# Performance work log

Hardware: AMD Instinct MI355X
Metric: run time of the kernel (lower is better)

The kernel has to match this reference:

```python
import jax, jax.numpy as jnp
import numpy as np

K, B, L, D_IN, H = 4, 16, 4096, 512, 128

def setup_inputs() -> dict:
    key = jax.random.key(0)
    k1, k2, k3, k4, k5 = jax.random.split(key, 5)
    hs = jax.random.normal(k1, (K, B, L, D_IN), dtype=jnp.float32)
    mask = jax.random.randint(k2, (B, L), 0, 2, dtype=jnp.int32)
    # xavier-ish scaled params
    ln_w = jax.random.normal(k3, (H, D_IN + H), dtype=jnp.float32) * (1.0 / np.sqrt(D_IN + H))
    ln_b = jnp.zeros((H,), dtype=jnp.float32)
    v_w = jax.random.normal(k4, (H,), dtype=jnp.float32) * (1.0 / np.sqrt(H))
    vq = jax.random.normal(k5, (H,), dtype=jnp.float32) * (1.0 / np.sqrt(H))
    return {"hs": hs, "mask": mask, "ln_w": ln_w, "ln_b": ln_b, "v_w": v_w, "vq": vq}

def reference(hs, mask, ln_w, ln_b, v_w, vq):
    # hs: [K,B,L,D], mask: [B,L], ln_w: [H, D+H], vq/v_w/ln_b: [H]
    d = hs.shape[-1]
    W_h = ln_w[:, :d]        # [H, D]
    W_q = ln_w[:, d:]        # [H, H]
    # Linear over concat([hs, vq]) == hs @ W_h.T + W_q @ vq + b (vq is constant per position)
    q_bias = W_q @ vq + ln_b                      # [H]
    h = jnp.tanh(jnp.einsum('kbld,hd->kblh', hs, W_h) + q_bias)
    s = jnp.einsum('kblh,h->kbl', h, v_w)         # [K,B,L]
    s = s - (mask[None] == 0).astype(s.dtype) * 10000.0
    a = jax.nn.softmax(s, axis=0)                 # softmax over the K (stack) axis
    x = jnp.einsum('kbl,kbld->bld', a, hs)        # weighted sum over K
    return x  # dropout is identity in eval mode
```

## Files before the change

### kernel.cpp

```cpp
#include <hip/hip_runtime.h>
#include <hip/hip_bf16.h>
#include <stdint.h>

#define KK 4
#define BB 16
#define LL 4096
#define DD 512
#define HH 128

typedef __attribute__((ext_vector_type(8))) short bf16x8;
typedef __attribute__((ext_vector_type(4))) float f32x4;
typedef __attribute__((ext_vector_type(4))) unsigned int u32x4;

__device__ __forceinline__ unsigned int pack_bf16(float lo, float hi) {
  unsigned int a = __float_as_uint(lo);
  unsigned int b = __float_as_uint(hi);
  a = (a + 0x7FFFu + ((a >> 16) & 1u)) >> 16;
  b = (b + 0x7FFFu + ((b >> 16) & 1u)) >> 16;
  return a | (b << 16);
}

__device__ __forceinline__ void bar_lds() {
  __builtin_amdgcn_sched_barrier(0);
  asm volatile("s_waitcnt lgkmcnt(0)" ::: "memory");
  __builtin_amdgcn_s_barrier();
  __builtin_amdgcn_sched_barrier(0);
}

__global__ void qbias_kernel(const float* __restrict__ ln_w,
                             const float* __restrict__ ln_b,
                             const float* __restrict__ vq,
                             float* __restrict__ qb) {
  int h = threadIdx.x;
  if (h < HH) {
    float acc = ln_b[h];
    const float* wq = ln_w + (size_t)h * (DD + HH) + DD;
    for (int j = 0; j < HH; ++j) acc = fmaf(wq[j], vq[j], acc);
    qb[h] = acc;
  }
}

__global__ void wf_kernel(const float* __restrict__ ln_w,
                          unsigned int* __restrict__ wf) {
  int gid = blockIdx.x * 256 + threadIdx.x;
  int ks = gid >> 9;
  int nt = (gid >> 6) & 7;
  int lane = gid & 63;
  int h = nt * 16 + (lane & 15);
  int d0 = ks * 32 + (lane >> 4) * 8;
  const float* src = ln_w + (size_t)h * (DD + HH) + d0;
  u32x4 v;
  v.x = pack_bf16(src[0], src[1]);
  v.y = pack_bf16(src[2], src[3]);
  v.z = pack_bf16(src[4], src[5]);
  v.w = pack_bf16(src[6], src[7]);
  *(u32x4*)(wf + (size_t)gid * 4) = v;
}

__global__ __launch_bounds__(512) void agg_main(
    const float* __restrict__ hs, const unsigned int* __restrict__ wf,
    const float* __restrict__ qb, const float* __restrict__ vw,
    float* __restrict__ out) {
  extern __shared__ char smem[];
  char* abuf = smem;
  f32x4* spv = (f32x4*)(smem + 65536);

  const int tid = threadIdx.x;
  const int lane = tid & 63;
  const int wv = tid >> 6;
  const int r = lane & 15;
  const int cg = lane >> 4;

  const int b = blockIdx.x >> 4;
  const int l0b = (blockIdx.x & 15) << 8;

  bf16x8 wreg[16];
#pragma unroll
  for (int ks = 0; ks < 16; ++ks)
    wreg[ks] = *(const bf16x8*)(wf + ((size_t)((ks * 8 + wv) * 64 + lane)) * 4);

  const float qbr = qb[wv * 16 + r];
  const float vwr = vw[wv * 16 + r];

  f32x4 sv[8];
  auto issue_stage = [&](int l0) {
#pragma unroll
    for (int i = 0; i < 4; ++i) {
      int row = i * 8 + wv;
      int k = row & 3, pos = row >> 2;
      int d0 = (lane ^ (row & 7)) * 8;
      const float* p = hs + (((size_t)(k * BB + b)) * LL + l0 + pos) * DD + d0;
      sv[i * 2]     = *(const f32x4*)(p);
      sv[i * 2 + 1] = *(const f32x4*)(p + 4);
    }
  };
  auto write_stage = [&](char* dst) {
#pragma unroll
    for (int i = 0; i < 4; ++i) {
      u32x4 pk;
      pk.x = pack_bf16(sv[i * 2].x, sv[i * 2].y);
      pk.y = pack_bf16(sv[i * 2].z, sv[i * 2].w);
      pk.z = pack_bf16(sv[i * 2 + 1].x, sv[i * 2 + 1].y);
      pk.w = pack_bf16(sv[i * 2 + 1].z, sv[i * 2 + 1].w);
      *(u32x4*)(dst + i * 8192 + tid * 16) = pk;
    }
  };

  issue_stage(l0b);
  write_stage(abuf);
  bar_lds();

  for (int t = 0; t < 32; ++t) {
    const int l0 = l0b + t * 8;
    char* cur = abuf + (t & 1) * 32768;
    char* nxt = abuf + ((t & 1) ^ 1) * 32768;

    if (t < 31) issue_stage(l0 + 8);

    f32x4 acc0 = {0.f, 0.f, 0.f, 0.f};
    f32x4 acc1 = {0.f, 0.f, 0.f, 0.f};
    const int swz = (r & 7) << 4;
#pragma unroll
    for (int ks = 0; ks < 16; ++ks) {
      int inner = (ks * 64 + cg * 16) ^ swz;
      bf16x8 a0 = *(const bf16x8*)(cur + r * 1024 + inner);
      bf16x8 a1 = *(const bf16x8*)(cur + (16 + r) * 1024 + inner);
      acc0 = __builtin_amdgcn_mfma_f32_16x16x32_bf16(a0, wreg[ks], acc0, 0, 0, 0);
      acc1 = __builtin_amdgcn_mfma_f32_16x16x32_bf16(a1, wreg[ks], acc1, 0, 0, 0);
    }

    float ps[8];
#pragma unroll
    for (int st = 0; st < 2; ++st) {
      f32x4 acc = st ? acc1 : acc0;
#pragma unroll
      for (int j = 0; j < 4; ++j) {
        float z = acc[j] + qbr;
        z = fminf(15.f, fmaxf(-15.f, z));
        float e = __expf(-2.f * z);
        float th = (1.f - e) * __builtin_amdgcn_rcpf(1.f + e);
        ps[st * 4 + j] = vwr * th;
      }
    }
#pragma unroll
    for (int m = 1; m < 16; m <<= 1) {
#pragma unroll
      for (int q = 0; q < 8; ++q) ps[q] += __shfl_xor(ps[q], m, 64);
    }
    if (r == 0) {
      f32x4 v0 = {ps[0], ps[1], ps[2], ps[3]};
      f32x4 v1 = {ps[4], ps[5], ps[6], ps[7]};
      spv[cg * 8 + wv] = v0;
      spv[(4 + cg) * 8 + wv] = v1;
    }
    bar_lds();

    float a0, a1, a2, a3;
    {
      f32x4 s = spv[wv * 8 + 0];
#pragma unroll
      for (int w2 = 1; w2 < 8; ++w2) s += spv[wv * 8 + w2];
      float mx = fmaxf(fmaxf(s.x, s.y), fmaxf(s.z, s.w));
      float e0 = __expf(s.x - mx), e1 = __expf(s.y - mx);
      float e2 = __expf(s.z - mx), e3 = __expf(s.w - mx);
      float inv = __builtin_amdgcn_rcpf(e0 + e1 + e2 + e3);
      a0 = e0 * inv; a1 = e1 * inv; a2 = e2 * inv; a3 = e3 * inv;
    }

    {
      float x[8];
#pragma unroll
      for (int j = 0; j < 8; ++j) x[j] = 0.f;
#pragma unroll
      for (int k = 0; k < 4; ++k) {
        int row = wv * 4 + k;
        float ak = k == 0 ? a0 : (k == 1 ? a1 : (k == 2 ? a2 : a3));
        u32x4 u = *(const u32x4*)(cur + row * 1024 + ((lane * 16) ^ ((row & 7) << 4)));
        x[0] = fmaf(ak, __uint_as_float(u.x << 16), x[0]);
        x[1] = fmaf(ak, __uint_as_float(u.x & 0xffff0000u), x[1]);
        x[2] = fmaf(ak, __uint_as_float(u.y << 16), x[2]);
        x[3] = fmaf(ak, __uint_as_float(u.y & 0xffff0000u), x[3]);
        x[4] = fmaf(ak, __uint_as_float(u.z << 16), x[4]);
        x[5] = fmaf(ak, __uint_as_float(u.z & 0xffff0000u), x[5]);
        x[6] = fmaf(ak, __uint_as_float(u.w << 16), x[6]);
        x[7] = fmaf(ak, __uint_as_float(u.w & 0xffff0000u), x[7]);
      }
      float* ob = out + (((size_t)b) * LL + l0 + wv) * DD + lane * 8;
      f32x4 o0 = {x[0], x[1], x[2], x[3]};
      f32x4 o1 = {x[4], x[5], x[6], x[7]};
      *(f32x4*)(ob) = o0;
      *(f32x4*)(ob + 4) = o1;
    }

    if (t < 31) write_stage(nxt);
    bar_lds();
  }
}

extern "C" void kernel_launch(void* const* d_in, const int* in_sizes, int n_in,
                              void* d_out, int out_size, void* d_ws, size_t ws_size,
                              hipStream_t stream) {
  const float* hs   = (const float*)d_in[0];
  const float* ln_w = (const float*)d_in[2];
  const float* ln_b = (const float*)d_in[3];
  const float* v_w  = (const float*)d_in[4];
  const float* vq   = (const float*)d_in[5];
  float* out = (float*)d_out;

  unsigned int* wf = (unsigned int*)d_ws;
  float* qb = (float*)((char*)d_ws + 131072);

  qbias_kernel<<<1, 128, 0, stream>>>(ln_w, ln_b, vq, qb);
  wf_kernel<<<32, 256, 0, stream>>>(ln_w, wf);
  agg_main<<<256, 512, 66560, stream>>>(hs, wf, qb, v_w, out);
}
```

Measured before the change: 151.5 us.

## Repartition MFMA work so each wave shares A loads across two H tiles

Each wave now computes one 16-row M tile against two 16-column H tiles instead of two M tiles against one H tile. Each A fragment is loaded from LDS once and reused for two MFMAs, and the pre-tanh work is folded so each wave reduces 4 partial sums, not 8. Other changes: the 16-lane reduction uses DPP row_shr adds instead of shfl_xor, the hs rows for the weighted sum are loaded from LDS before the barrier, and output stores are nontemporal. The cost is doubled weight registers (32 bf16x8 per lane), which may raise register pressure and lower occupancy.

```diff
diff --git a/kernel.cpp b/kernel.cpp
--- a/kernel.cpp
+++ b/kernel.cpp
@@ -25,6 +25,13 @@
   asm volatile("s_waitcnt lgkmcnt(0)" ::: "memory");
   __builtin_amdgcn_s_barrier();
   __builtin_amdgcn_sched_barrier(0);
+}
+
+template <int N>
+__device__ __forceinline__ float dpp_shr_add(float x) {
+  int y = __builtin_amdgcn_update_dpp(0, __float_as_int(x), 0x110 | N, 0xF, 0xF,
+                                      true);
+  return x + __int_as_float(y);
 }
 
 __global__ void qbias_kernel(const float* __restrict__ ln_w,
@@ -70,17 +77,22 @@
   const int wv = tid >> 6;
   const int r = lane & 15;
   const int cg = lane >> 4;
+  const int st = wv & 1;
+  const int p2 = wv >> 1;
+  const int ntA = p2 * 2, ntB = ntA + 1;
 
   const int b = blockIdx.x >> 4;
   const int l0b = (blockIdx.x & 15) << 8;
 
-  bf16x8 wreg[16];
-#pragma unroll
-  for (int ks = 0; ks < 16; ++ks)
-    wreg[ks] = *(const bf16x8*)(wf + ((size_t)((ks * 8 + wv) * 64 + lane)) * 4);
-
-  const float qbr = qb[wv * 16 + r];
-  const float vwr = vw[wv * 16 + r];
+  bf16x8 wregA[16], wregB[16];
+#pragma unroll
+  for (int ks = 0; ks < 16; ++ks) {
+    wregA[ks] = *(const bf16x8*)(wf + ((size_t)((ks * 8 + ntA) * 64 + lane)) * 4);
+    wregB[ks] = *(const bf16x8*)(wf + ((size_t)((ks * 8 + ntB) * 64 + lane)) * 4);
+  }
+
+  const float qbrA = qb[ntA * 16 + r], qbrB = qb[ntB * 16 + r];
+  const float vwrA = vw[ntA * 16 + r], vwrB = vw[ntB * 16 + r];
 
   f32x4 sv[8];
   auto issue_stage = [&](int l0) {
@@ -117,49 +129,56 @@
 
     if (t < 31) issue_stage(l0 + 8);
 
-    f32x4 acc0 = {0.f, 0.f, 0.f, 0.f};
-    f32x4 acc1 = {0.f, 0.f, 0.f, 0.f};
+    f32x4 accA = {0.f, 0.f, 0.f, 0.f};
+    f32x4 accB = {0.f, 0.f, 0.f, 0.f};
+    const int arow = (st * 16 + r) * 1024;
     const int swz = (r & 7) << 4;
 #pragma unroll
     for (int ks = 0; ks < 16; ++ks) {
-      int inner = (ks * 64 + cg * 16) ^ swz;
-      bf16x8 a0 = *(const bf16x8*)(cur + r * 1024 + inner);
-      bf16x8 a1 = *(const bf16x8*)(cur + (16 + r) * 1024 + inner);
-      acc0 = __builtin_amdgcn_mfma_f32_16x16x32_bf16(a0, wreg[ks], acc0, 0, 0, 0);
-      acc1 = __builtin_amdgcn_mfma_f32_16x16x32_bf16(a1, wreg[ks], acc1, 0, 0, 0);
-    }
-
-    float ps[8];
-#pragma unroll
-    for (int st = 0; st < 2; ++st) {
-      f32x4 acc = st ? acc1 : acc0;
-#pragma unroll
-      for (int j = 0; j < 4; ++j) {
-        float z = acc[j] + qbr;
-        z = fminf(15.f, fmaxf(-15.f, z));
-        float e = __expf(-2.f * z);
-        float th = (1.f - e) * __builtin_amdgcn_rcpf(1.f + e);
-        ps[st * 4 + j] = vwr * th;
-      }
-    }
-#pragma unroll
-    for (int m = 1; m < 16; m <<= 1) {
-#pragma unroll
-      for (int q = 0; q < 8; ++q) ps[q] += __shfl_xor(ps[q], m, 64);
-    }
-    if (r == 0) {
-      f32x4 v0 = {ps[0], ps[1], ps[2], ps[3]};
-      f32x4 v1 = {ps[4], ps[5], ps[6], ps[7]};
-      spv[cg * 8 + wv] = v0;
-      spv[(4 + cg) * 8 + wv] = v1;
+      bf16x8 a = *(const bf16x8*)(cur + arow + ((ks * 64 + cg * 16) ^ swz));
+      accA = __builtin_amdgcn_mfma_f32_16x16x32_bf16(a, wregA[ks], accA, 0, 0, 0);
+      accB = __builtin_amdgcn_mfma_f32_16x16x32_bf16(a, wregB[ks], accB, 0, 0, 0);
+    }
+
+    u32x4 uu[4];
+#pragma unroll
+    for (int k = 0; k < 4; ++k) {
+      int row = wv * 4 + k;
+      uu[k] = *(const u32x4*)(cur + row * 1024 + ((lane * 16) ^ ((row & 7) << 4)));
+    }
+
+    float ps[4];
+#pragma unroll
+    for (int j = 0; j < 4; ++j) {
+      float zA = accA[j] + qbrA;
+      zA = fminf(15.f, fmaxf(-15.f, zA));
+      float eA = __expf(-2.f * zA);
+      float thA = (1.f - eA) * __builtin_amdgcn_rcpf(1.f + eA);
+      float zB = accB[j] + qbrB;
+      zB = fminf(15.f, fmaxf(-15.f, zB));
+      float eB = __expf(-2.f * zB);
+      float thB = (1.f - eB) * __builtin_amdgcn_rcpf(1.f + eB);
+      ps[j] = fmaf(vwrA, thA, vwrB * thB);
+    }
+#pragma unroll
+    for (int j = 0; j < 4; ++j) {
+      ps[j] = dpp_shr_add<1>(ps[j]);
+      ps[j] = dpp_shr_add<2>(ps[j]);
+      ps[j] = dpp_shr_add<4>(ps[j]);
+      ps[j] = dpp_shr_add<8>(ps[j]);
+    }
+    if (r == 15) {
+      f32x4 v = {ps[0], ps[1], ps[2], ps[3]};
+      spv[(st * 4 + cg) * 4 + p2] = v;
     }
     bar_lds();
 
     float a0, a1, a2, a3;
     {
-      f32x4 s = spv[wv * 8 + 0];
-#pragma unroll
-      for (int w2 = 1; w2 < 8; ++w2) s += spv[wv * 8 + w2];
+      f32x4 s = spv[wv * 4 + 0];
+      s += spv[wv * 4 + 1];
+      s += spv[wv * 4 + 2];
+      s += spv[wv * 4 + 3];
       float mx = fmaxf(fmaxf(s.x, s.y), fmaxf(s.z, s.w));
       float e0 = __expf(s.x - mx), e1 = __expf(s.y - mx);
       float e2 = __expf(s.z - mx), e3 = __expf(s.w - mx);
@@ -173,9 +192,8 @@
       for (int j = 0; j < 8; ++j) x[j] = 0.f;
 #pragma unroll
       for (int k = 0; k < 4; ++k) {
-        int row = wv * 4 + k;
         float ak = k == 0 ? a0 : (k == 1 ? a1 : (k == 2 ? a2 : a3));
-        u32x4 u = *(const u32x4*)(cur + row * 1024 + ((lane * 16) ^ ((row & 7) << 4)));
+        u32x4 u = uu[k];
         x[0] = fmaf(ak, __uint_as_float(u.x << 16), x[0]);
         x[1] = fmaf(ak, __uint_as_float(u.x & 0xffff0000u), x[1]);
         x[2] = fmaf(ak, __uint_as_float(u.y << 16), x[2]);
@@ -188,8 +206,8 @@
       float* ob = out + (((size_t)b) * LL + l0 + wv) * DD + lane * 8;
       f32x4 o0 = {x[0], x[1], x[2], x[3]};
       f32x4 o1 = {x[4], x[5], x[6], x[7]};
-      *(f32x4*)(ob) = o0;
-      *(f32x4*)(ob + 4) = o1;
+      __builtin_nontemporal_store(o0, (f32x4*)ob);
+      __builtin_nontemporal_store(o1, (f32x4*)(ob + 4));
     }
 
     if (t < 31) write_stage(nxt);
@@ -212,5 +230,5 @@
 
   qbias_kernel<<<1, 128, 0, stream>>>(ln_w, ln_b, vq, qb);
   wf_kernel<<<32, 256, 0, stream>>>(ln_w, wf);
-  agg_main<<<256, 512, 66560, stream>>>(hs, wf, qb, v_w, out);
-}
+  agg_main<<<256, 512, 66048, stream>>>(hs, wf, qb, v_w, out);
+}
```

Result: no change. 151.4 us (-0.1%).

## Deepen global-load prefetch to two stages, use DPP reductions and nontemporal stores

Applied to the files above, without the earlier changes.

The main loop is unrolled by two with two register staging sets, so global loads for stage t+2 are issued while stage t+1's data is written to LDS. The aim is to keep more hs loads in flight and hide HBM latency. The cross-lane score reduction now uses DPP row_shr adds instead of xor shuffles, with the result read from lane 15 instead of lane 0. Output stores are marked nontemporal to avoid polluting cache. The second register set raises register pressure, which could reduce occupancy or cause spills.

```diff
diff --git a/kernel.cpp b/kernel.cpp
--- a/kernel.cpp
+++ b/kernel.cpp
@@ -25,6 +25,13 @@
   asm volatile("s_waitcnt lgkmcnt(0)" ::: "memory");
   __builtin_amdgcn_s_barrier();
   __builtin_amdgcn_sched_barrier(0);
+}
+
+template <int N>
+__device__ __forceinline__ float dpp_shr_add(float x) {
+  int y = __builtin_amdgcn_update_dpp(0, __float_as_int(x), 0x110 | N, 0xF, 0xF,
+                                      true);
+  return x + __int_as_float(y);
 }
 
 __global__ void qbias_kernel(const float* __restrict__ ln_w,
@@ -62,7 +69,8 @@
     const float* __restrict__ qb, const float* __restrict__ vw,
     float* __restrict__ out) {
   extern __shared__ char smem[];
-  char* abuf = smem;
+  char* buf0 = smem;
+  char* buf1 = smem + 32768;
   f32x4* spv = (f32x4*)(smem + 65536);
 
   const int tid = threadIdx.x;
@@ -82,8 +90,7 @@
   const float qbr = qb[wv * 16 + r];
   const float vwr = vw[wv * 16 + r];
 
-  f32x4 sv[8];
-  auto issue_stage = [&](int l0) {
+  auto issue_stage = [&](int l0, f32x4* sv) {
 #pragma unroll
     for (int i = 0; i < 4; ++i) {
       int row = i * 8 + wv;
@@ -94,7 +101,7 @@
       sv[i * 2 + 1] = *(const f32x4*)(p + 4);
     }
   };
-  auto write_stage = [&](char* dst) {
+  auto write_stage = [&](char* dst, const f32x4* sv) {
 #pragma unroll
     for (int i = 0; i < 4; ++i) {
       u32x4 pk;
@@ -106,16 +113,9 @@
     }
   };
 
-  issue_stage(l0b);
-  write_stage(abuf);
-  bar_lds();
-
-  for (int t = 0; t < 32; ++t) {
-    const int l0 = l0b + t * 8;
-    char* cur = abuf + (t & 1) * 32768;
-    char* nxt = abuf + ((t & 1) ^ 1) * 32768;
-
-    if (t < 31) issue_stage(l0 + 8);
+  auto body = [&](int l0, char* cur, char* nxt, const f32x4* svWr, f32x4* svIs,
+                  bool doIssue, bool doWrite) {
+    if (doIssue) issue_stage(l0 + 16, svIs);
 
     f32x4 acc0 = {0.f, 0.f, 0.f, 0.f};
     f32x4 acc1 = {0.f, 0.f, 0.f, 0.f};
@@ -143,14 +143,16 @@
       }
     }
 #pragma unroll
-    for (int m = 1; m < 16; m <<= 1) {
-#pragma unroll
-      for (int q = 0; q < 8; ++q) ps[q] += __shfl_xor(ps[q], m, 64);
-    }
-    if (r == 0) {
+    for (int q = 0; q < 8; ++q) {
+      ps[q] = dpp_shr_add<1>(ps[q]);
+      ps[q] = dpp_shr_add<2>(ps[q]);
+      ps[q] = dpp_shr_add<4>(ps[q]);
+      ps[q] = dpp_shr_add<8>(ps[q]);
+    }
+    if (r == 15) {
       f32x4 v0 = {ps[0], ps[1], ps[2], ps[3]};
       f32x4 v1 = {ps[4], ps[5], ps[6], ps[7]};
-      spv[cg * 8 + wv] = v0;
+      spv[(0 + cg) * 8 + wv] = v0;
       spv[(4 + cg) * 8 + wv] = v1;
     }
     bar_lds();
@@ -175,7 +177,8 @@
       for (int k = 0; k < 4; ++k) {
         int row = wv * 4 + k;
         float ak = k == 0 ? a0 : (k == 1 ? a1 : (k == 2 ? a2 : a3));
-        u32x4 u = *(const u32x4*)(cur + row * 1024 + ((lane * 16) ^ ((row & 7) << 4)));
+        u32x4 u = *(const u32x4*)(cur + row * 1024 +
+                                  ((lane * 16) ^ ((row & 7) << 4)));
         x[0] = fmaf(ak, __uint_as_float(u.x << 16), x[0]);
         x[1] = fmaf(ak, __uint_as_float(u.x & 0xffff0000u), x[1]);
         x[2] = fmaf(ak, __uint_as_float(u.y << 16), x[2]);
@@ -188,12 +191,26 @@
       float* ob = out + (((size_t)b) * LL + l0 + wv) * DD + lane * 8;
       f32x4 o0 = {x[0], x[1], x[2], x[3]};
       f32x4 o1 = {x[4], x[5], x[6], x[7]};
-      *(f32x4*)(ob) = o0;
-      *(f32x4*)(ob + 4) = o1;
-    }
-
-    if (t < 31) write_stage(nxt);
+      __builtin_nontemporal_store(o0, (f32x4*)ob);
+      __builtin_nontemporal_store(o1, (f32x4*)(ob + 4));
+    }
+
+    if (doWrite) write_stage(nxt, svWr);
     bar_lds();
+  };
+
+  f32x4 svA[8], svB[8];
+
+  issue_stage(l0b, svA);
+  write_stage(buf0, svA);
+  issue_stage(l0b + 8, svA);
+  bar_lds();
+
+  for (int tt = 0; tt < 16; ++tt) {
+    const int l0 = l0b + tt * 16;
+    const bool more = (tt < 15);
+    body(l0, buf0, buf1, svA, svB, more, true);
+    body(l0 + 8, buf1, buf0, svB, svA, more, more);
   }
 }
 
```

New measurement: 147.2 us. 2.8% less time.
